# Kernel optimization log

Hardware: AMD Instinct MI355X
Metric: run time of the kernel (lower is better)

## Reference

```python
import jax, jax.numpy as jnp
import numpy as np

N_NODES = 100_000
N_EDGES = 1_000_000
N_GRAPHS = 2048
F_IN, N_HEADS, HEAD_DIM = 128, 2, 32
NEG_SLOPE = 0.2


def seg_softmax(logits, seg, num):
    # numerically stable scatter-softmax over segments (leading axis)
    m = jax.ops.segment_max(logits, seg, num_segments=num)
    e = jnp.exp(logits - m[seg])
    s = jax.ops.segment_sum(e, seg, num_segments=num)
    return e / s[seg]


def setup_inputs() -> dict:
    key = jax.random.key(0)
    ks = jax.random.split(key, 10)
    HC = N_HEADS * HEAD_DIM
    x = jax.random.normal(ks[0], (N_NODES, F_IN), jnp.float32)
    edge_index = jax.random.randint(ks[1], (2, N_EDGES), 0, N_NODES, jnp.int32)
    batch = jnp.sort(jax.random.randint(ks[2], (N_NODES,), 0, N_GRAPHS, jnp.int32))
    sc_in = 1.0 / np.sqrt(F_IN)
    sc_hc = 1.0 / np.sqrt(HC)
    W_l = jax.random.normal(ks[3], (F_IN, HC), jnp.float32) * sc_in
    W_r = jax.random.normal(ks[4], (F_IN, HC), jnp.float32) * sc_in
    att = jax.random.normal(ks[5], (N_HEADS, HEAD_DIM), jnp.float32) * (1.0 / np.sqrt(HEAD_DIM))
    bias = jnp.zeros((HC,), jnp.float32)
    w_rel = jax.random.normal(ks[6], (HC,), jnp.float32) * sc_hc
    w_root = jax.random.normal(ks[7], (HC,), jnp.float32) * sc_hc
    b_score = jnp.zeros((1,), jnp.float32)
    return {"x": x, "edge_index": edge_index, "batch": batch, "W_l": W_l,
            "W_r": W_r, "att": att, "bias": bias, "w_rel": w_rel,
            "w_root": w_root, "b_score": b_score}


def reference(x, edge_index, batch, W_l, W_r, att, bias, w_rel, w_root, b_score):
    N = x.shape[0]
    H, C = att.shape
    src, dst = edge_index[0], edge_index[1]
    # --- GATv2Conv (add_self_loops=True, concat heads, negative_slope=0.2) ---
    loop = jnp.arange(N, dtype=src.dtype)
    s = jnp.concatenate([src, loop])  # source j
    d = jnp.concatenate([dst, loop])  # target i
    xl = (x @ W_l).reshape(N, H, C)   # lin_l -> source features
    xr = (x @ W_r).reshape(N, H, C)   # lin_r -> target features
    e = jax.nn.leaky_relu(xl[s] + xr[d], NEG_SLOPE)       # [E', H, C]
    logits = jnp.einsum('ehc,hc->eh', e, att)              # [E', H]
    alpha = seg_softmax(logits, d, N)                      # softmax over incoming edges per target
    h = jax.ops.segment_sum(xl[s] * alpha[:, :, None], d, num_segments=N)
    h = h.reshape(N, H * C) + bias                         # conv output (data.x)
    # --- SAGPooling(min_score=-1): softmax(GraphConv score) keeps all nodes ---
    aggr = jax.ops.segment_sum(h[src], dst, num_segments=N)  # GraphConv neighbor add-aggr
    score = aggr @ w_rel + h @ w_root + b_score              # [N]
    sm = seg_softmax(score, batch, N_GRAPHS)
    px = h * sm[:, None]
    # --- global_add_pool + global_mean_pool ---
    add = jax.ops.segment_sum(px, batch, num_segments=N_GRAPHS)
    cnt = jax.ops.segment_sum(jnp.ones((N,), px.dtype), batch, num_segments=N_GRAPHS)
    mean = add / jnp.maximum(cnt, 1.0)[:, None]
    return add + mean  # global_emb [N_GRAPHS, H*C]
```

## Files before the change

### kernel.cpp

```cpp
#include <hip/hip_runtime.h>
#include <hip/hip_bf16.h>

#define N_NODES 100000
#define N_EDGES 1000000
#define N_GRAPHS 2048
#define F_IN 128
#define NEG_SLOPE 0.2f
#define E_TOT (N_EDGES + N_NODES)
#define GEMM_BLOCKS 782
#define NODE_BLOCKS 391
#define NB 1563
#define EB 269
#define EB_PAD 272
#define CPW_BLOCKS 391

typedef short  bf16x8 __attribute__((ext_vector_type(8)));
typedef float  f32x16 __attribute__((ext_vector_type(16)));

__device__ __forceinline__ short f2bf(float f) {
    unsigned u = __float_as_uint(f);
    unsigned r = (u + 0x7fffu + ((u >> 16) & 1u)) >> 16;
    return (short)r;
}
__device__ __forceinline__ float bf2f(short h) {
    return __uint_as_float(((unsigned)(unsigned short)h) << 16);
}

template <int CTRL>
__device__ __forceinline__ float dpp_add(float x) {
    return x + __int_as_float(__builtin_amdgcn_update_dpp(
        0, __float_as_int(x), CTRL, 0xf, 0xf, true));
}
__device__ __forceinline__ float full_sum64(float x) {
    x = dpp_add<0x111>(x);
    x = dpp_add<0x112>(x);
    x = dpp_add<0x114>(x);
    x = dpp_add<0x118>(x);
    x = dpp_add<0x142>(x);
    x = dpp_add<0x143>(x);
    return x;
}
__device__ __forceinline__ float quad_sum(float x) {
    x = dpp_add<0xB1>(x);
    x = dpp_add<0x4E>(x);
    return x;
}
__device__ __forceinline__ float red8(float x) {
    x = dpp_add<0x128>(x);
    x += __shfl_xor(x, 16, 64);
    x += __shfl_xor(x, 32, 64);
    return x;
}

__global__ __launch_bounds__(256) void k_gemm_bhist(const float* __restrict__ x,
                                                    const float* __restrict__ Wl,
                                                    const float* __restrict__ Wr,
                                                    const int* __restrict__ ei,
                                                    float* __restrict__ xr,
                                                    short* __restrict__ xlb,
                                                    int* __restrict__ bhist) {
    __shared__ unsigned char smem[2 * 128 * 136 * 2];
    int tid = threadIdx.x;
    if (blockIdx.x >= GEMM_BLOCKS) {
        int* lh = (int*)smem;
        int b = blockIdx.x - GEMM_BLOCKS;
        for (int i = tid; i < NB; i += 256) lh[i] = 0;
        __syncthreads();
        int e0 = b * 4096;
#pragma unroll
        for (int j = 0; j < 16; ++j) {
            int e = e0 + j * 256 + tid;
            if (e < E_TOT) {
                int d = (e < N_EDGES) ? ei[N_EDGES + e] : (e - N_EDGES);
                atomicAdd(&lh[d >> 6], 1);
            }
        }
        __syncthreads();
        for (int i = tid; i < NB; i += 256)
            bhist[(size_t)i * EB_PAD + b] = lh[i];
        return;
    }
    typedef short wt_t[128][136];
    wt_t* wt = (wt_t*)smem;
    {
        int k  = tid >> 1;
        int cq = tid & 1;
        const float* Wsrc = cq ? Wr : Wl;
#pragma unroll
        for (int u = 0; u < 16; ++u) {
            int c0 = u * 4;
            float4 wv = *(const float4*)(Wsrc + (size_t)k * 64 + c0);
            float vv[4] = {wv.x, wv.y, wv.z, wv.w};
#pragma unroll
            for (int q = 0; q < 4; ++q) {
                int c = cq * 64 + c0 + q;
                short hi = f2bf(vv[q]);
                wt[0][c][k] = hi;
                wt[1][c][k] = f2bf(vv[q] - bf2f(hi));
            }
        }
    }
    __syncthreads();
    int lane = tid & 63, w = tid >> 6;
    int m = lane & 31, half = lane >> 5;
    int row = blockIdx.x * 128 + w * 32 + m;
    bool rv = row < N_NODES;
    const float* xrow = x + (size_t)(rv ? row : 0) * F_IN;
    f32x16 acc[4];
#pragma unroll
    for (int t = 0; t < 4; ++t)
#pragma unroll
        for (int i = 0; i < 16; ++i) acc[t][i] = 0.f;

#pragma unroll
    for (int kt = 0; kt < 8; ++kt) {
        int kb = kt * 16 + half * 8;
        float4 xa = rv ? *(const float4*)(xrow + kb)
                       : make_float4(0.f, 0.f, 0.f, 0.f);
        float4 xb = rv ? *(const float4*)(xrow + kb + 4)
                       : make_float4(0.f, 0.f, 0.f, 0.f);
        float xs[8] = {xa.x, xa.y, xa.z, xa.w, xb.x, xb.y, xb.z, xb.w};
        bf16x8 ahi, alo;
#pragma unroll
        for (int j = 0; j < 8; ++j) {
            short hi = f2bf(xs[j]);
            ahi[j] = hi;
            alo[j] = f2bf(xs[j] - bf2f(hi));
        }
#pragma unroll
        for (int t = 0; t < 4; ++t) {
            int n = t * 32 + m;
            bf16x8 bhi = *(const bf16x8*)&wt[0][n][kb];
            bf16x8 blo = *(const bf16x8*)&wt[1][n][kb];
            acc[t] = __builtin_amdgcn_mfma_f32_32x32x16_bf16(ahi, bhi, acc[t], 0, 0, 0);
            acc[t] = __builtin_amdgcn_mfma_f32_32x32x16_bf16(ahi, blo, acc[t], 0, 0, 0);
            acc[t] = __builtin_amdgcn_mfma_f32_32x32x16_bf16(alo, bhi, acc[t], 0, 0, 0);
        }
    }
    int r0 = blockIdx.x * 128 + w * 32 + 4 * half;
#pragma unroll
    for (int t = 0; t < 4; ++t)
#pragma unroll
        for (int reg = 0; reg < 16; ++reg) {
            int rr = r0 + (reg & 3) + 8 * (reg >> 2);
            if (rr < N_NODES) {
                if (t < 2)
                    xlb[(size_t)rr * 64 + t * 32 + m] = f2bf(acc[t][reg]);
                else
                    xr[(size_t)rr * 64 + (t - 2) * 32 + m] = acc[t][reg];
            }
        }
}

__global__ __launch_bounds__(256) void k_colprefix_bounds(int* __restrict__ bhist,
                                                          int* __restrict__ colsum,
                                                          const int* __restrict__ batch,
                                                          int* __restrict__ start) {
    if (blockIdx.x < CPW_BLOCKS) {
        int wv = blockIdx.x * 4 + (threadIdx.x >> 6);
        if (wv >= NB) return;
        int lane = threadIdx.x & 63;
        int* row = bhist + (size_t)wv * EB_PAD;
        int carry = 0;
        for (int base = 0; base < EB; base += 64) {
            int idx = base + lane;
            int v = (idx < EB) ? row[idx] : 0;
            int inc = v;
#pragma unroll
            for (int o = 1; o < 64; o <<= 1) {
                int t = __shfl_up(inc, o, 64);
                if (lane >= o) inc += t;
            }
            int tot = __shfl(inc, 63, 64);
            if (idx < EB) row[idx] = carry + inc - v;
            carry += tot;
        }
        if (lane == 0) colsum[wv] = carry;
    } else {
        int i = (blockIdx.x - CPW_BLOCKS) * 256 + threadIdx.x;
        if (i >= N_NODES) return;
        int bi = batch[i];
        int bp = (i == 0) ? -1 : batch[i - 1];
        for (int g = bp + 1; g <= bi; ++g) start[g] = i;
        if (i == N_NODES - 1)
            for (int g = bi + 1; g <= N_GRAPHS; ++g) start[g] = N_NODES;
    }
}

__global__ __launch_bounds__(256) void k_bscatter(const int* __restrict__ ei,
                                                  const int* __restrict__ bhist,
                                                  const int* __restrict__ colsum,
                                                  int* __restrict__ colbase,
                                                  int* __restrict__ bpack) {
    __shared__ int lh[NB];
    __shared__ int cb[NB + 1];
    __shared__ int sctmp[256];
    int tid = threadIdx.x, b = blockIdx.x;
    {
        int v[7]; int s = 0;
#pragma unroll
        for (int k = 0; k < 7; ++k) {
            int idx = tid * 7 + k;
            v[k] = (idx < NB) ? colsum[idx] : 0;
            s += v[k];
        }
        sctmp[tid] = s; __syncthreads();
        for (int off = 1; off < 256; off <<= 1) {
            int xv = (tid >= off) ? sctmp[tid - off] : 0;
            __syncthreads();
            sctmp[tid] += xv;
            __syncthreads();
        }
        int run = sctmp[tid] - s;
#pragma unroll
        for (int k = 0; k < 7; ++k) {
            int idx = tid * 7 + k;
            if (idx <= NB) cb[idx] = run;
            run += v[k];
        }
    }
    for (int i = tid; i < NB; i += 256) lh[i] = 0;
    __syncthreads();
    if (b == 0)
        for (int i = tid; i <= NB; i += 256) colbase[i] = cb[i];
    int e0 = b * 4096;
#pragma unroll
    for (int j = 0; j < 16; ++j) {
        int e = e0 + j * 256 + tid;
        if (e < E_TOT) {
            int s, d;
            if (e < N_EDGES) { s = ei[e]; d = ei[N_EDGES + e]; }
            else             { s = d = e - N_EDGES; }
            int bk = d >> 6;
            int lr = atomicAdd(&lh[bk], 1);
            int pos = cb[bk] + bhist[(size_t)bk * EB_PAD + b] + lr;
            bpack[pos] = s | ((d & 63) << 17);
        }
    }
}

__global__ __launch_bounds__(256) void k_fine(const int* __restrict__ bpack,
                                              const int* __restrict__ colbase,
                                              int* __restrict__ rowptr,
                                              int* __restrict__ sorted_src) {
    __shared__ int fcnt[64];
    __shared__ int foff[64];
    int i = blockIdx.x, tid = threadIdx.x;
    if (i == 0 && tid < 16) sorted_src[E_TOT + tid] = 0;
    int cb0 = colbase[i], cb1 = colbase[i + 1];
    if (tid < 64) fcnt[tid] = 0;
    __syncthreads();
    for (int e = cb0 + tid; e < cb1; e += 256)
        atomicAdd(&fcnt[bpack[e] >> 17], 1);
    __syncthreads();
    if (tid < 64) {
        int v = fcnt[tid];
        int inc = v;
#pragma unroll
        for (int o = 1; o < 64; o <<= 1) {
            int t = __shfl_up(inc, o, 64);
            if (tid >= o) inc += t;
        }
        int excl = inc - v;
        foff[tid] = excl;
        int node = i * 64 + tid;
        if (node <= N_NODES) rowptr[node] = cb0 + excl;
    }
    __syncthreads();
    for (int e = cb0 + tid; e < cb1; e += 256) {
        int w = bpack[e];
        int lr = atomicAdd(&foff[w >> 17], 1);
        sorted_src[cb0 + lr] = w & 131071;
    }
}

__device__ __forceinline__ void gat_edge8(bf16x8 xb, bool valid,
                                          const float* __restrict__ xr8,
                                          const float* __restrict__ att8,
                                          float& wsum, float* __restrict__ acc8) {
    float xv[8];
#pragma unroll
    for (int j = 0; j < 8; ++j) xv[j] = bf2f(xb[j]);
    float p = 0.f;
#pragma unroll
    for (int j = 0; j < 8; ++j) {
        float v = xv[j] + xr8[j];
        v = fmaxf(v, NEG_SLOPE * v);
        p += v * att8[j];
    }
    p = quad_sum(p);
    float w = valid ? __expf(p) : 0.f;
    wsum += w;
#pragma unroll
    for (int j = 0; j < 8; ++j) acc8[j] += w * xv[j];
}

__global__ __launch_bounds__(256) void k_gat(const short* __restrict__ xlb,
                                             const float* __restrict__ xr,
                                             const int* __restrict__ rowptr,
                                             const int* __restrict__ sorted_src,
                                             const float* __restrict__ att,
                                             const float* __restrict__ bias,
                                             const float* __restrict__ w_rel,
                                             const float* __restrict__ w_root,
                                             float* __restrict__ hfeat,
                                             float* __restrict__ tbuf,
                                             float* __restrict__ rbuf) {
    int lane = threadIdx.x & 63;
    int du0 = __builtin_amdgcn_readfirstlane(blockIdx.x * 8 + (threadIdx.x >> 6) * 2);
    int du1 = du0 + 1;
    int grp = lane >> 3, sub = lane & 7;
    float xrA[8], xrB[8], att8[8];
    {
        float4 a = *(const float4*)(xr + (size_t)du0 * 64 + sub * 8);
        float4 b = *(const float4*)(xr + (size_t)du0 * 64 + sub * 8 + 4);
        float4 e = *(const float4*)(xr + (size_t)du1 * 64 + sub * 8);
        float4 f = *(const float4*)(xr + (size_t)du1 * 64 + sub * 8 + 4);
        xrA[0]=a.x; xrA[1]=a.y; xrA[2]=a.z; xrA[3]=a.w;
        xrA[4]=b.x; xrA[5]=b.y; xrA[6]=b.z; xrA[7]=b.w;
        xrB[0]=e.x; xrB[1]=e.y; xrB[2]=e.z; xrB[3]=e.w;
        xrB[4]=f.x; xrB[5]=f.y; xrB[6]=f.z; xrB[7]=f.w;
        float4 c = *(const float4*)(att + sub * 8);
        float4 d = *(const float4*)(att + sub * 8 + 4);
        att8[0]=c.x; att8[1]=c.y; att8[2]=c.z; att8[3]=c.w;
        att8[4]=d.x; att8[5]=d.y; att8[6]=d.z; att8[7]=d.w;
    }
    int j0a = __builtin_amdgcn_readfirstlane(rowptr[du0]);
    int j1a = __builtin_amdgcn_readfirstlane(rowptr[du0 + 1]);
    int j1b = __builtin_amdgcn_readfirstlane(rowptr[du0 + 2]);
    int j0b = j1a;
    float wsA = 0.f, wsB = 0.f;
    float accA[8] = {0.f,0.f,0.f,0.f,0.f,0.f,0.f,0.f};
    float accB[8] = {0.f,0.f,0.f,0.f,0.f,0.f,0.f,0.f};
    int ita = j0a, itb = j0b;
    while (ita < j1a || itb < j1b) {
        bool dA = ita < j1a, dB = itb < j1b;
        bool dA2 = false, dB2 = false;
        int jA0 = 0, jB0 = 0;
        bf16x8 a0, a1, b0, b1;
        if (dA) {
            jA0 = ita + grp;
            int c0 = (jA0 > j1a - 1) ? j1a - 1 : jA0;
            int s0 = sorted_src[c0];
            a0 = *(const bf16x8*)(xlb + (size_t)(unsigned)s0 * 64 + sub * 8);
            dA2 = (ita + 8 < j1a);
            if (dA2) {
                int c1 = (jA0 + 8 > j1a - 1) ? j1a - 1 : jA0 + 8;
                int s1 = sorted_src[c1];
                a1 = *(const bf16x8*)(xlb + (size_t)(unsigned)s1 * 64 + sub * 8);
            }
        }
        if (dB) {
            jB0 = itb + grp;
            int c0 = (jB0 > j1b - 1) ? j1b - 1 : jB0;
            int s0 = sorted_src[c0];
            b0 = *(const bf16x8*)(xlb + (size_t)(unsigned)s0 * 64 + sub * 8);
            dB2 = (itb + 8 < j1b);
            if (dB2) {
                int c1 = (jB0 + 8 > j1b - 1) ? j1b - 1 : jB0 + 8;
                int s1 = sorted_src[c1];
                b1 = *(const bf16x8*)(xlb + (size_t)(unsigned)s1 * 64 + sub * 8);
            }
        }
        if (dA) {
            gat_edge8(a0, jA0 < j1a, xrA, att8, wsA, accA);
            if (dA2) gat_edge8(a1, jA0 + 8 < j1a, xrA, att8, wsA, accA);
        }
        if (dB) {
            gat_edge8(b0, jB0 < j1b, xrB, att8, wsB, accB);
            if (dB2) gat_edge8(b1, jB0 + 8 < j1b, xrB, att8, wsB, accB);
        }
        ita += 16; itb += 16;
    }
    float4 bi0 = *(const float4*)(bias + sub * 8);
    float4 bi1 = *(const float4*)(bias + sub * 8 + 4);
    float4 wr0 = *(const float4*)(w_rel + sub * 8);
    float4 wr1 = *(const float4*)(w_rel + sub * 8 + 4);
    float4 wo0 = *(const float4*)(w_root + sub * 8);
    float4 wo1 = *(const float4*)(w_root + sub * 8 + 4);
    wsA = red8(wsA);
    wsB = red8(wsB);
#pragma unroll
    for (int j = 0; j < 8; ++j) { accA[j] = red8(accA[j]); accB[j] = red8(accB[j]); }
    float invA = 1.0f / wsA;
    float invB = 1.0f / wsB;
    float bi8[8] = {bi0.x, bi0.y, bi0.z, bi0.w, bi1.x, bi1.y, bi1.z, bi1.w};
    float hA[8], hB[8];
#pragma unroll
    for (int j = 0; j < 8; ++j) {
        hA[j] = fmaf(accA[j], invA, bi8[j]);
        hB[j] = fmaf(accB[j], invB, bi8[j]);
    }
    if (grp == 0) {
        float4 s0 = make_float4(hA[0], hA[1], hA[2], hA[3]);
        float4 s1 = make_float4(hA[4], hA[5], hA[6], hA[7]);
        *(float4*)(hfeat + (size_t)du0 * 64 + sub * 8)     = s0;
        *(float4*)(hfeat + (size_t)du0 * 64 + sub * 8 + 4) = s1;
    } else if (grp == 1) {
        float4 s0 = make_float4(hB[0], hB[1], hB[2], hB[3]);
        float4 s1 = make_float4(hB[4], hB[5], hB[6], hB[7]);
        *(float4*)(hfeat + (size_t)du1 * 64 + sub * 8)     = s0;
        *(float4*)(hfeat + (size_t)du1 * 64 + sub * 8 + 4) = s1;
    }
    float wrel8[8]  = {wr0.x, wr0.y, wr0.z, wr0.w, wr1.x, wr1.y, wr1.z, wr1.w};
    float wroot8[8] = {wo0.x, wo0.y, wo0.z, wo0.w, wo1.x, wo1.y, wo1.z, wo1.w};
    float aA = 0.f, bA = 0.f, aB = 0.f, bB = 0.f;
#pragma unroll
    for (int j = 0; j < 8; ++j) {
        aA += hA[j] * wrel8[j];
        bA += hA[j] * wroot8[j];
        aB += hB[j] * wrel8[j];
        bB += hB[j] * wroot8[j];
    }
    aA = full_sum64(aA) * 0.125f;
    bA = full_sum64(bA) * 0.125f;
    aB = full_sum64(aB) * 0.125f;
    bB = full_sum64(bB) * 0.125f;
    if (lane == 63) {
        tbuf[du0] = aA; rbuf[du0] = bA;
        tbuf[du1] = aB; rbuf[du1] = bB;
    }
}

__global__ __launch_bounds__(256) void k_pool(const int* __restrict__ rowptr,
                                              const int* __restrict__ sorted_src,
                                              const float* __restrict__ t,
                                              const float* __restrict__ r,
                                              const float* __restrict__ b_score,
                                              float* __restrict__ score,
                                              const float* __restrict__ h,
                                              const int* __restrict__ start,
                                              float* __restrict__ out) {
    __shared__ float sh[4];
    __shared__ float shacc[4][64];
    int g = blockIdx.x;
    int tid = threadIdx.x, w = tid >> 6, lane = tid & 63;
    int n0 = start[g], n1 = start[g + 1];
    int cnt = n1 - n0;
    if (cnt <= 0) { if (tid < 64) out[(size_t)g * 64 + tid] = 0.f; return; }
    float bsc = b_score[0];
    for (int base = n0; base < n1; base += 64) {
        int i = base + (tid >> 2);
        float sum = 0.f;
        int jj0 = 0, jj1 = 0;
        if (i < n1) { jj0 = rowptr[i]; jj1 = rowptr[i + 1]; }
        for (int j = jj0 + (tid & 3); j < jj1; j += 4)
            sum += t[sorted_src[j]];
        sum = quad_sum(sum);
        if (i < n1 && (tid & 3) == 0)
            score[i] = sum - t[i] + r[i] + bsc;
    }
    __syncthreads();
    float m = -1e30f;
    for (int i = n0 + tid; i < n1; i += 256) m = fmaxf(m, score[i]);
#pragma unroll
    for (int o = 32; o; o >>= 1) m = fmaxf(m, __shfl_xor(m, o, 64));
    if (lane == 0) sh[w] = m;
    __syncthreads();
    m = fmaxf(fmaxf(sh[0], sh[1]), fmaxf(sh[2], sh[3]));
    __syncthreads();
    float ssum = 0.f;
    for (int i = n0 + tid; i < n1; i += 256) {
        float e = __expf(score[i] - m);
        score[i] = e;
        ssum += e;
    }
#pragma unroll
    for (int o = 32; o; o >>= 1) ssum += __shfl_xor(ssum, o, 64);
    if (lane == 0) sh[w] = ssum;
    __syncthreads();
    ssum = sh[0] + sh[1] + sh[2] + sh[3];
    float acc = 0.f;
    for (int i = n0 + w; i < n1; i += 4)
        acc += score[i] * h[(size_t)i * 64 + lane];
    shacc[w][lane] = acc;
    __syncthreads();
    if (w == 0) {
        float tot = shacc[0][lane] + shacc[1][lane] + shacc[2][lane] + shacc[3][lane];
        out[(size_t)g * 64 + lane] = tot * (1.f + 1.f / (float)cnt) / ssum;
    }
}

extern "C" void kernel_launch(void* const* d_in, const int* in_sizes, int n_in,
                              void* d_out, int out_size, void* d_ws, size_t ws_size,
                              hipStream_t stream) {
    const float* x      = (const float*)d_in[0];
    const int*   ei     = (const int*)d_in[1];
    const int*   batch  = (const int*)d_in[2];
    const float* Wl     = (const float*)d_in[3];
    const float* Wr     = (const float*)d_in[4];
    const float* att    = (const float*)d_in[5];
    const float* bias   = (const float*)d_in[6];
    const float* w_rel  = (const float*)d_in[7];
    const float* w_root = (const float*)d_in[8];
    const float* b_sc   = (const float*)d_in[9];

    char* ws = (char*)d_ws;
    size_t off = 0;
    auto alloc = [&](size_t bytes) { void* p = ws + off; off += (bytes + 255) & ~255ull; return p; };
    float* xr         = (float*)alloc((size_t)N_NODES * 64 * 4);
    short* xlb        = (short*)alloc((size_t)N_NODES * 64 * 2);
    float* hfeat      = (float*)alloc((size_t)N_NODES * 64 * 4);
    int*   bhist      = (int*)hfeat;
    int*   bpack      = (int*)  alloc((size_t)E_TOT * 4);
    int*   sorted_src = (int*)  alloc((size_t)(E_TOT + 16) * 4);
    int*   rowptr     = (int*)  alloc((size_t)(N_NODES + 1) * 4);
    int*   colsum     = (int*)  alloc((size_t)NB * 4);
    int*   colbase    = (int*)  alloc((size_t)(NB + 1) * 4);
    float* tbuf       = (float*)alloc((size_t)N_NODES * 4);
    float* rbuf       = (float*)alloc((size_t)N_NODES * 4);
    float* score      = (float*)alloc((size_t)N_NODES * 4);
    int*   start      = (int*)  alloc((size_t)(N_GRAPHS + 1) * 4);

    k_gemm_bhist      <<<GEMM_BLOCKS + EB, 256, 0, stream>>>(x, Wl, Wr, ei, xr, xlb, bhist);
    k_colprefix_bounds<<<CPW_BLOCKS + NODE_BLOCKS, 256, 0, stream>>>(bhist, colsum, batch, start);
    k_bscatter        <<<EB, 256, 0, stream>>>(ei, bhist, colsum, colbase, bpack);
    k_fine            <<<NB, 256, 0, stream>>>(bpack, colbase, rowptr, sorted_src);
    k_gat             <<<N_NODES / 8, 256, 0, stream>>>(xlb, xr, rowptr, sorted_src, att, bias,
                                                        w_rel, w_root, hfeat, tbuf, rbuf);
    k_pool            <<<N_GRAPHS, 256, 0, stream>>>(rowptr, sorted_src, tbuf, rbuf, b_sc,
                                                     score, hfeat, start, (float*)d_out);
}
```

Measured before the change: 225.9 us.

## Build CSR with a single cooperative kernel using global atomics

Replaces the two-level bucket sort CSR construction (block histograms, column prefix, bucket scatter, fine sort) with one cooperative-groups kernel. That kernel counts per-node in-degree with global atomics, scans the degrees, and scatters source indices through per-node atomic cursors, with grid-wide syncs between phases. This cuts several kernel launches and intermediate buffers. In exchange it brings random global atomics and scattered writes, and grid.sync overhead. The edge histogram also no longer overlaps with the GEMM. The zero-padding of the tail of sorted_src is dropped, which could matter if the GAT kernel reads past the edge count.

Measured after the change: 815.1 us. 261% more time.

```diff
diff --git a/kernel.cpp b/kernel.cpp
--- a/kernel.cpp
+++ b/kernel.cpp
@@ -1,5 +1,8 @@
 #include <hip/hip_runtime.h>
 #include <hip/hip_bf16.h>
+#include <hip/hip_cooperative_groups.h>
+
+namespace cg = cooperative_groups;
 
 #define N_NODES 100000
 #define N_EDGES 1000000
@@ -9,10 +12,7 @@
 #define E_TOT (N_EDGES + N_NODES)
 #define GEMM_BLOCKS 782
 #define NODE_BLOCKS 391
-#define NB 1563
-#define EB 269
-#define EB_PAD 272
-#define CPW_BLOCKS 391
+#define KC_BLOCKS 1024
 
 typedef short  bf16x8 __attribute__((ext_vector_type(8)));
 typedef float  f32x16 __attribute__((ext_vector_type(16)));
@@ -52,34 +52,13 @@
     return x;
 }
 
-__global__ __launch_bounds__(256) void k_gemm_bhist(const float* __restrict__ x,
-                                                    const float* __restrict__ Wl,
-                                                    const float* __restrict__ Wr,
-                                                    const int* __restrict__ ei,
-                                                    float* __restrict__ xr,
-                                                    short* __restrict__ xlb,
-                                                    int* __restrict__ bhist) {
+__global__ __launch_bounds__(256) void k_gemm(const float* __restrict__ x,
+                                              const float* __restrict__ Wl,
+                                              const float* __restrict__ Wr,
+                                              float* __restrict__ xr,
+                                              short* __restrict__ xlb) {
     __shared__ unsigned char smem[2 * 128 * 136 * 2];
     int tid = threadIdx.x;
-    if (blockIdx.x >= GEMM_BLOCKS) {
-        int* lh = (int*)smem;
-        int b = blockIdx.x - GEMM_BLOCKS;
-        for (int i = tid; i < NB; i += 256) lh[i] = 0;
-        __syncthreads();
-        int e0 = b * 4096;
-#pragma unroll
-        for (int j = 0; j < 16; ++j) {
-            int e = e0 + j * 256 + tid;
-            if (e < E_TOT) {
-                int d = (e < N_EDGES) ? ei[N_EDGES + e] : (e - N_EDGES);
-                atomicAdd(&lh[d >> 6], 1);
-            }
-        }
-        __syncthreads();
-        for (int i = tid; i < NB; i += 256)
-            bhist[(size_t)i * EB_PAD + b] = lh[i];
-        return;
-    }
     typedef short wt_t[128][136];
     wt_t* wt = (wt_t*)smem;
     {
@@ -152,19 +131,51 @@
         }
 }
 
-__global__ __launch_bounds__(256) void k_colprefix_bounds(int* __restrict__ bhist,
-                                                          int* __restrict__ colsum,
-                                                          const int* __restrict__ batch,
-                                                          int* __restrict__ start) {
-    if (blockIdx.x < CPW_BLOCKS) {
-        int wv = blockIdx.x * 4 + (threadIdx.x >> 6);
-        if (wv >= NB) return;
-        int lane = threadIdx.x & 63;
-        int* row = bhist + (size_t)wv * EB_PAD;
+__global__ __launch_bounds__(256) void k_csr(const int* __restrict__ ei,
+                                             const int* __restrict__ batch,
+                                             int* __restrict__ deg,
+                                             int* __restrict__ bsum,
+                                             int* __restrict__ bbase,
+                                             int* __restrict__ rowptr,
+                                             int* __restrict__ cursor,
+                                             int* __restrict__ sorted_src,
+                                             int* __restrict__ start) {
+    cg::grid_group grid = cg::this_grid();
+    __shared__ int sctmp[256];
+    int tid = threadIdx.x;
+    int gtid = blockIdx.x * 256 + tid;
+    const int gstride = KC_BLOCKS * 256;
+    for (int i = gtid; i < N_NODES; i += gstride) {
+        deg[i] = 0;
+        int bi = batch[i];
+        int bp = (i == 0) ? -1 : batch[i - 1];
+        for (int g = bp + 1; g <= bi; ++g) start[g] = i;
+        if (i == N_NODES - 1)
+            for (int g = bi + 1; g <= N_GRAPHS; ++g) start[g] = N_NODES;
+    }
+    grid.sync();
+    for (int e = gtid; e < E_TOT; e += gstride) {
+        int d = (e < N_EDGES) ? ei[N_EDGES + e] : (e - N_EDGES);
+        atomicAdd(&deg[d], 1);
+    }
+    grid.sync();
+    if (blockIdx.x < NODE_BLOCKS) {
+        int i = blockIdx.x * 256 + tid;
+        int v = (i < N_NODES) ? deg[i] : 0;
+        int s = v;
+#pragma unroll
+        for (int o = 1; o < 64; o <<= 1) s += __shfl_xor(s, o, 64);
+        if ((tid & 63) == 0) sctmp[tid >> 6] = s;
+        __syncthreads();
+        if (tid == 0) bsum[blockIdx.x] = sctmp[0] + sctmp[1] + sctmp[2] + sctmp[3];
+    }
+    grid.sync();
+    if (blockIdx.x == 0 && tid < 64) {
+        int lane = tid;
         int carry = 0;
-        for (int base = 0; base < EB; base += 64) {
+        for (int base = 0; base < NODE_BLOCKS; base += 64) {
             int idx = base + lane;
-            int v = (idx < EB) ? row[idx] : 0;
+            int v = (idx < NODE_BLOCKS) ? bsum[idx] : 0;
             int inc = v;
 #pragma unroll
             for (int o = 1; o < 64; o <<= 1) {
@@ -172,105 +183,33 @@
                 if (lane >= o) inc += t;
             }
             int tot = __shfl(inc, 63, 64);
-            if (idx < EB) row[idx] = carry + inc - v;
+            if (idx < NODE_BLOCKS) bbase[idx] = carry + inc - v;
             carry += tot;
         }
-        if (lane == 0) colsum[wv] = carry;
-    } else {
-        int i = (blockIdx.x - CPW_BLOCKS) * 256 + threadIdx.x;
-        if (i >= N_NODES) return;
-        int bi = batch[i];
-        int bp = (i == 0) ? -1 : batch[i - 1];
-        for (int g = bp + 1; g <= bi; ++g) start[g] = i;
-        if (i == N_NODES - 1)
-            for (int g = bi + 1; g <= N_GRAPHS; ++g) start[g] = N_NODES;
-    }
-}
-
-__global__ __launch_bounds__(256) void k_bscatter(const int* __restrict__ ei,
-                                                  const int* __restrict__ bhist,
-                                                  const int* __restrict__ colsum,
-                                                  int* __restrict__ colbase,
-                                                  int* __restrict__ bpack) {
-    __shared__ int lh[NB];
-    __shared__ int cb[NB + 1];
-    __shared__ int sctmp[256];
-    int tid = threadIdx.x, b = blockIdx.x;
-    {
-        int v[7]; int s = 0;
-#pragma unroll
-        for (int k = 0; k < 7; ++k) {
-            int idx = tid * 7 + k;
-            v[k] = (idx < NB) ? colsum[idx] : 0;
-            s += v[k];
-        }
-        sctmp[tid] = s; __syncthreads();
+    }
+    grid.sync();
+    if (blockIdx.x < NODE_BLOCKS) {
+        int i = blockIdx.x * 256 + tid;
+        int v = (i < N_NODES) ? deg[i] : 0;
+        sctmp[tid] = v;
+        __syncthreads();
         for (int off = 1; off < 256; off <<= 1) {
             int xv = (tid >= off) ? sctmp[tid - off] : 0;
             __syncthreads();
             sctmp[tid] += xv;
             __syncthreads();
         }
-        int run = sctmp[tid] - s;
-#pragma unroll
-        for (int k = 0; k < 7; ++k) {
-            int idx = tid * 7 + k;
-            if (idx <= NB) cb[idx] = run;
-            run += v[k];
-        }
-    }
-    for (int i = tid; i < NB; i += 256) lh[i] = 0;
-    __syncthreads();
-    if (b == 0)
-        for (int i = tid; i <= NB; i += 256) colbase[i] = cb[i];
-    int e0 = b * 4096;
-#pragma unroll
-    for (int j = 0; j < 16; ++j) {
-        int e = e0 + j * 256 + tid;
-        if (e < E_TOT) {
-            int s, d;
-            if (e < N_EDGES) { s = ei[e]; d = ei[N_EDGES + e]; }
-            else             { s = d = e - N_EDGES; }
-            int bk = d >> 6;
-            int lr = atomicAdd(&lh[bk], 1);
-            int pos = cb[bk] + bhist[(size_t)bk * EB_PAD + b] + lr;
-            bpack[pos] = s | ((d & 63) << 17);
-        }
-    }
-}
-
-__global__ __launch_bounds__(256) void k_fine(const int* __restrict__ bpack,
-                                              const int* __restrict__ colbase,
-                                              int* __restrict__ rowptr,
-                                              int* __restrict__ sorted_src) {
-    __shared__ int fcnt[64];
-    __shared__ int foff[64];
-    int i = blockIdx.x, tid = threadIdx.x;
-    if (i == 0 && tid < 16) sorted_src[E_TOT + tid] = 0;
-    int cb0 = colbase[i], cb1 = colbase[i + 1];
-    if (tid < 64) fcnt[tid] = 0;
-    __syncthreads();
-    for (int e = cb0 + tid; e < cb1; e += 256)
-        atomicAdd(&fcnt[bpack[e] >> 17], 1);
-    __syncthreads();
-    if (tid < 64) {
-        int v = fcnt[tid];
-        int inc = v;
-#pragma unroll
-        for (int o = 1; o < 64; o <<= 1) {
-            int t = __shfl_up(inc, o, 64);
-            if (tid >= o) inc += t;
-        }
-        int excl = inc - v;
-        foff[tid] = excl;
-        int node = i * 64 + tid;
-        if (node <= N_NODES) rowptr[node] = cb0 + excl;
-    }
-    __syncthreads();
-    for (int e = cb0 + tid; e < cb1; e += 256) {
-        int w = bpack[e];
-        int lr = atomicAdd(&foff[w >> 17], 1);
-        sorted_src[cb0 + lr] = w & 131071;
+        int excl = sctmp[tid] - v + bbase[blockIdx.x];
+        if (i < N_NODES) { rowptr[i] = excl; cursor[i] = excl; }
+        if (gtid == 0) rowptr[N_NODES] = E_TOT;
+    }
+    grid.sync();
+    for (int e = gtid; e < E_TOT; e += gstride) {
+        int s, d;
+        if (e < N_EDGES) { s = ei[e]; d = ei[N_EDGES + e]; }
+        else             { s = d = e - N_EDGES; }
+        int pos = atomicAdd(&cursor[d], 1);
+        sorted_src[pos] = s;
     }
 }
 
@@ -501,23 +440,29 @@
     float* xr         = (float*)alloc((size_t)N_NODES * 64 * 4);
     short* xlb        = (short*)alloc((size_t)N_NODES * 64 * 2);
     float* hfeat      = (float*)alloc((size_t)N_NODES * 64 * 4);
-    int*   bhist      = (int*)hfeat;
-    int*   bpack      = (int*)  alloc((size_t)E_TOT * 4);
     int*   sorted_src = (int*)  alloc((size_t)(E_TOT + 16) * 4);
     int*   rowptr     = (int*)  alloc((size_t)(N_NODES + 1) * 4);
-    int*   colsum     = (int*)  alloc((size_t)NB * 4);
-    int*   colbase    = (int*)  alloc((size_t)(NB + 1) * 4);
+    int*   cursor     = (int*)  alloc((size_t)N_NODES * 4);
+    int*   deg        = (int*)  alloc((size_t)N_NODES * 4);
+    int*   bsum       = (int*)  alloc((size_t)NODE_BLOCKS * 4);
+    int*   bbase      = (int*)  alloc((size_t)NODE_BLOCKS * 4);
     float* tbuf       = (float*)alloc((size_t)N_NODES * 4);
     float* rbuf       = (float*)alloc((size_t)N_NODES * 4);
     float* score      = (float*)alloc((size_t)N_NODES * 4);
     int*   start      = (int*)  alloc((size_t)(N_GRAPHS + 1) * 4);
 
-    k_gemm_bhist      <<<GEMM_BLOCKS + EB, 256, 0, stream>>>(x, Wl, Wr, ei, xr, xlb, bhist);
-    k_colprefix_bounds<<<CPW_BLOCKS + NODE_BLOCKS, 256, 0, stream>>>(bhist, colsum, batch, start);
-    k_bscatter        <<<EB, 256, 0, stream>>>(ei, bhist, colsum, colbase, bpack);
-    k_fine            <<<NB, 256, 0, stream>>>(bpack, colbase, rowptr, sorted_src);
-    k_gat             <<<N_NODES / 8, 256, 0, stream>>>(xlb, xr, rowptr, sorted_src, att, bias,
-                                                        w_rel, w_root, hfeat, tbuf, rbuf);
-    k_pool            <<<N_GRAPHS, 256, 0, stream>>>(rowptr, sorted_src, tbuf, rbuf, b_sc,
-                                                     score, hfeat, start, (float*)d_out);
-}
+    k_gemm<<<GEMM_BLOCKS, 256, 0, stream>>>(x, Wl, Wr, xr, xlb);
+
+    {
+        void* kcArgs[] = {(void*)&ei, (void*)&batch, (void*)&deg, (void*)&bsum,
+                          (void*)&bbase, (void*)&rowptr, (void*)&cursor,
+                          (void*)&sorted_src, (void*)&start};
+        hipLaunchCooperativeKernel((const void*)k_csr, dim3(KC_BLOCKS), dim3(256),
+                                   kcArgs, 0, stream);
+    }
+
+    k_gat <<<N_NODES / 8, 256, 0, stream>>>(xlb, xr, rowptr, sorted_src, att, bias,
+                                            w_rel, w_root, hfeat, tbuf, rbuf);
+    k_pool<<<N_GRAPHS, 256, 0, stream>>>(rowptr, sorted_src, tbuf, rbuf, b_sc,
+                                         score, hfeat, start, (float*)d_out);
+}
```
